# Performance work log

Measured on AMD Instinct MI355X. Metric: run time of the kernel, lower is better.

Reference implementation:

```python
import jax, jax.numpy as jnp
import numpy as np

B, N = 4, 1024            # batches, atoms per structure
IN_CH, OUT_CH = 16, 16
N_BASIS = 16
MAX_RADIUS = 3.5
BOX_L = 19.7              # cubic lattice constant -> ~24 neighbors/atom
GAMMA = MAX_RADIUS / N_BASIS
N_NORM = 24.0             # avg neighbor count, out /= sqrt(n_norm)


def _build_periodic_edges(seed=0):
    rng = np.random.default_rng(seed)
    pos = rng.uniform(0.0, BOX_L, (B, N, 3)).astype(np.float32)
    shifts = BOX_L * np.array([[i, j, k] for i in (-1, 0, 1)
                               for j in (-1, 0, 1) for k in (-1, 0, 1)],
                              dtype=np.float32)
    src_l, dst_l, vec_l = [], [], []
    r2 = MAX_RADIUS * MAX_RADIUS
    for z in range(B):
        p = pos[z]
        for s in shifts:  # 27 periodic images, chunked to keep memory small
            diff = (p[None, :, :] + s[None, None, :]) - p[:, None, :]  # [a,b,3] = image_b - a
            d2 = (diff * diff).sum(-1)
            a_idx, b_idx = np.nonzero(d2 < r2)
            dst_l.append((z * N + a_idx).astype(np.int32))
            src_l.append((z * N + b_idx).astype(np.int32))
            vec_l.append(diff[a_idx, b_idx])
    edge_src = np.concatenate(src_l)
    edge_dst = np.concatenate(dst_l)
    edge_vec = np.concatenate(vec_l).astype(np.float32)
    # original zeroes self-image displacements with |r| < 1e-10
    self_mask = np.linalg.norm(edge_vec, axis=-1) < 1e-10
    edge_vec[self_mask] = 0.0
    return edge_src, edge_dst, edge_vec


def setup_inputs() -> dict:
    key = jax.random.key(0)
    k1, k2 = jax.random.split(key)
    edge_src, edge_dst, edge_vec = _build_periodic_edges()
    x = jax.random.normal(k1, (B * N, IN_CH), dtype=jnp.float32)
    W = jax.random.normal(k2, (N_BASIS + 3, OUT_CH, IN_CH), dtype=jnp.float32) * 0.1
    return {
        "x": x,
        "W": W,
        "edge_vec": jnp.asarray(edge_vec),
        "edge_src": jnp.asarray(edge_src),
        "edge_dst": jnp.asarray(edge_dst),
    }


def reference(x, W, edge_vec, edge_src, edge_dst):
    # per-edge kernel features: gaussian radial basis + unit direction
    r = jnp.linalg.norm(edge_vec, axis=-1, keepdims=True)            # [E,1]
    centers = jnp.linspace(0.0, MAX_RADIUS, N_BASIS, dtype=x.dtype)
    basis = jnp.exp(-((r - centers) / GAMMA) ** 2)                   # [E,nb]
    rhat = jnp.where(r > 1e-10, edge_vec / jnp.maximum(r, 1e-10), 0.0)
    feat = jnp.concatenate([basis, rhat], axis=-1)                   # [E,nb+3]
    # per-edge kernel eval (kernels = self.kernel(radius) in the original)
    K = jnp.einsum('ef,foi->eoi', feat, W)                           # [E,out,in]
    # per-edge matvec + scatter-add over destination atoms
    msg = jnp.einsum('eoi,ei->eo', K, x[edge_src])                   # [E,out]
    out = jax.ops.segment_sum(msg, edge_dst, num_segments=x.shape[0])
    out = out / jnp.sqrt(jnp.asarray(N_NORM, x.dtype))               # n_norm ** 0.5
    return out.reshape(B, N, OUT_CH)
```

## Files before the change

kernel.cpp:

```cpp
#include <hip/hip_runtime.h>
#include <hip/hip_fp16.h>
#include <math.h>

#define IN_CH 16
#define OUT_CH 16
#define N_BASIS 16
#define N_FEAT 19
#define Y_STRIDE (N_FEAT * OUT_CH)
#define GAMMA_INV (16.0f / 3.5f)
#define CENTER_STEP (3.5f / 15.0f)
#define INV_SQRT_NNORM 0.20412414523193154f
#define APB 16
#define EPB 32

__global__ __launch_bounds__(320) void precompute_y(
    const float* __restrict__ x, const float* __restrict__ W,
    __half* __restrict__ y, float* __restrict__ out, int n_atoms) {
  __shared__ float xs[APB][IN_CH];
  const int t = threadIdx.x;
  const int a0 = blockIdx.x * APB;

  if (t < APB * IN_CH) {
    const int idx = a0 * IN_CH + t;
    const bool ok = idx < n_atoms * IN_CH;
    xs[t >> 4][t & 15] = ok ? x[idx] : 0.0f;
    if (ok) out[idx] = 0.0f;
  }

  float4 w0, w1, w2, w3;
  if (t < Y_STRIDE) {
    const float4* w4 = (const float4*)(W + t * IN_CH);
    w0 = w4[0]; w1 = w4[1]; w2 = w4[2]; w3 = w4[3];
  }
  __syncthreads();

  if (t < Y_STRIDE) {
#pragma unroll
    for (int al = 0; al < APB; ++al) {
      if (a0 + al >= n_atoms) break;
      const float* xv = xs[al];
      float acc = w0.x * xv[0] + w0.y * xv[1] + w0.z * xv[2] + w0.w * xv[3] +
                  w1.x * xv[4] + w1.y * xv[5] + w1.z * xv[6] + w1.w * xv[7] +
                  w2.x * xv[8] + w2.y * xv[9] + w2.z * xv[10] + w2.w * xv[11] +
                  w3.x * xv[12] + w3.y * xv[13] + w3.z * xv[14] + w3.w * xv[15];
      y[(size_t)(a0 + al) * Y_STRIDE + t] = __float2half(acc * INV_SQRT_NNORM);
    }
  }
}

__global__ __launch_bounds__(256) void edge_scatter(
    const __half* __restrict__ y, const float* __restrict__ edge_vec,
    const int* __restrict__ edge_src, const int* __restrict__ edge_dst,
    float* __restrict__ out, int E) {
  __shared__ float feat[EPB][20];
  __shared__ float msg[EPB][OUT_CH];
  __shared__ int dsts[EPB];

  const int t = threadIdx.x;
  const int w = t >> 7;
  const int rem = t & 127;
  const int el = rem & 15;
  const int h = rem >> 4;
  const int s = w * 16 + el;
  const int e = blockIdx.x * EPB + s;
  const bool valid = (e < E);

  float vx = 0.f, vy = 0.f, vz = 0.f;
  int src = 0;
  if (valid) {
    vx = edge_vec[3 * e + 0];
    vy = edge_vec[3 * e + 1];
    vz = edge_vec[3 * e + 2];
    src = edge_src[e];
    if (h == 0) dsts[s] = edge_dst[e];
  } else if (h == 0) {
    dsts[s] = -1 - s;
  }
  const float r = sqrtf(vx * vx + vy * vy + vz * vz);

  const float t0 = (r - CENTER_STEP * (float)(2 * h)) * GAMMA_INV;
  const float t1 = (r - CENTER_STEP * (float)(2 * h + 1)) * GAMMA_INV;
  feat[s][2 * h] = __expf(-t0 * t0);
  feat[s][2 * h + 1] = __expf(-t1 * t1);
  if (h < 3) {
    const float inv = (r > 1e-10f) ? (1.0f / r) : 0.0f;
    const float comp = (h == 0) ? vx : ((h == 1) ? vy : vz);
    feat[s][N_BASIS + h] = comp * inv;
  }
  __syncthreads();

  float a0 = 0.f, a1 = 0.f;
  if (valid) {
    const __half2* __restrict__ yrow =
        (const __half2*)(y + (size_t)src * Y_STRIDE + 2 * h);
#pragma unroll
    for (int f = 0; f < N_FEAT; ++f) {
      const float2 yv = __half22float2(yrow[f * (OUT_CH / 2)]);
      const float ff = feat[s][f];
      a0 += ff * yv.x;
      a1 += ff * yv.y;
    }
  }
  msg[s][2 * h] = a0;
  msg[s][2 * h + 1] = a1;
  __syncthreads();

  const int wb = w * 16;
  const int mydst = dsts[s];
  int leader = el;
#pragma unroll
  for (int k = 0; k < 16; ++k) {
    if (dsts[wb + k] == mydst) { leader = k; break; }
  }
  if (leader == el && mydst >= 0) {
    float s0 = 0.f, s1 = 0.f;
#pragma unroll
    for (int k = 0; k < 16; ++k) {
      if (k >= el && dsts[wb + k] == mydst) {
        s0 += msg[wb + k][2 * h];
        s1 += msg[wb + k][2 * h + 1];
      }
    }
    atomicAdd(&out[mydst * OUT_CH + 2 * h], s0);
    atomicAdd(&out[mydst * OUT_CH + 2 * h + 1], s1);
  }
}

__global__ __launch_bounds__(256) void edge_direct(
    const float* __restrict__ x, const float* __restrict__ W,
    const float* __restrict__ edge_vec, const int* __restrict__ edge_src,
    const int* __restrict__ edge_dst, float* __restrict__ out, int E) {
  __shared__ float Ws[N_FEAT * OUT_CH * IN_CH];
  __shared__ float feat[16][N_FEAT];
  __shared__ float xs[16][IN_CH];

  const int t = threadIdx.x;
  for (int i = t; i < N_FEAT * OUT_CH * IN_CH; i += 256) Ws[i] = W[i];

  const int eg = t >> 4;
  const int o = t & 15;
  const int e = blockIdx.x * 16 + eg;
  const bool valid = (e < E);

  float vx = 0.f, vy = 0.f, vz = 0.f;
  int src = 0, dst = 0;
  if (valid) {
    vx = edge_vec[3 * e + 0];
    vy = edge_vec[3 * e + 1];
    vz = edge_vec[3 * e + 2];
    src = edge_src[e];
    dst = edge_dst[e];
    xs[eg][o] = x[src * IN_CH + o];
  }
  const float r = sqrtf(vx * vx + vy * vy + vz * vz);
  const float tt = (r - CENTER_STEP * (float)o) * GAMMA_INV;
  feat[eg][o] = __expf(-tt * tt);
  if (o < 3) {
    const float inv = (r > 1e-10f) ? (1.0f / r) : 0.0f;
    const float comp = (o == 0) ? vx : ((o == 1) ? vy : vz);
    feat[eg][N_BASIS + o] = comp * inv;
  }
  __syncthreads();

  if (valid) {
    float acc = 0.f;
#pragma unroll
    for (int f = 0; f < N_FEAT; ++f) {
      const float* wrow = &Ws[(f * OUT_CH + o) * IN_CH];
      float dot = 0.f;
#pragma unroll
      for (int i = 0; i < IN_CH; ++i) dot += wrow[i] * xs[eg][i];
      acc += feat[eg][f] * dot;
    }
    atomicAdd(&out[dst * OUT_CH + o], acc * INV_SQRT_NNORM);
  }
}

extern "C" void kernel_launch(void* const* d_in, const int* in_sizes, int n_in,
                              void* d_out, int out_size, void* d_ws,
                              size_t ws_size, hipStream_t stream) {
  const float* x = (const float*)d_in[0];
  const float* W = (const float*)d_in[1];
  const float* edge_vec = (const float*)d_in[2];
  const int* edge_src = (const int*)d_in[3];
  const int* edge_dst = (const int*)d_in[4];
  float* out = (float*)d_out;

  const int E = in_sizes[3];
  const int n_atoms = in_sizes[0] / IN_CH;

  const size_t y_bytes = (size_t)n_atoms * Y_STRIDE * sizeof(__half);
  if (ws_size >= y_bytes) {
    __half* y = (__half*)d_ws;
    precompute_y<<<(n_atoms + APB - 1) / APB, 320, 0, stream>>>(x, W, y, out,
                                                               n_atoms);
    edge_scatter<<<(E + EPB - 1) / EPB, 256, 0, stream>>>(y, edge_vec, edge_src,
                                                          edge_dst, out, E);
  } else {
    hipMemsetAsync(out, 0, (size_t)out_size * sizeof(float), stream);
    edge_direct<<<(E + 15) / 16, 256, 0, stream>>>(x, W, edge_vec, edge_src,
                                                   edge_dst, out, E);
  }
}
```

Measured before the change: 90.31 us.

## Use one atom per block in precompute and remap edge_scatter thread layout

The precompute kernel now launches one block per atom instead of batching 16 atoms per block, so each block reloads the W row through global memory and uses less per-block reuse. In edge_scatter the thread-to-(edge, output pair) mapping is swapped so that the 8 output-pair threads of one edge are adjacent. The y-row reads per edge become contiguous within a wavefront, and messages are stored as float2. This trades better coalescing of the gathered y rows against more blocks and more redundant W loads in the precompute.

```diff
diff --git a/kernel.cpp b/kernel.cpp
--- a/kernel.cpp
+++ b/kernel.cpp
@@ -10,41 +10,29 @@
 #define GAMMA_INV (16.0f / 3.5f)
 #define CENTER_STEP (3.5f / 15.0f)
 #define INV_SQRT_NNORM 0.20412414523193154f
-#define APB 16
 #define EPB 32
 
 __global__ __launch_bounds__(320) void precompute_y(
     const float* __restrict__ x, const float* __restrict__ W,
-    __half* __restrict__ y, float* __restrict__ out, int n_atoms) {
-  __shared__ float xs[APB][IN_CH];
+    __half* __restrict__ y, float* __restrict__ out) {
+  __shared__ float xs[IN_CH];
+  const int a = blockIdx.x;
   const int t = threadIdx.x;
-  const int a0 = blockIdx.x * APB;
-
-  if (t < APB * IN_CH) {
-    const int idx = a0 * IN_CH + t;
-    const bool ok = idx < n_atoms * IN_CH;
-    xs[t >> 4][t & 15] = ok ? x[idx] : 0.0f;
-    if (ok) out[idx] = 0.0f;
+  if (t < IN_CH) {
+    xs[t] = x[a * IN_CH + t];
+    out[a * OUT_CH + t] = 0.0f;
   }
-
-  float4 w0, w1, w2, w3;
+  __syncthreads();
   if (t < Y_STRIDE) {
     const float4* w4 = (const float4*)(W + t * IN_CH);
-    w0 = w4[0]; w1 = w4[1]; w2 = w4[2]; w3 = w4[3];
-  }
-  __syncthreads();
-
-  if (t < Y_STRIDE) {
+    float acc = 0.f;
 #pragma unroll
-    for (int al = 0; al < APB; ++al) {
-      if (a0 + al >= n_atoms) break;
-      const float* xv = xs[al];
-      float acc = w0.x * xv[0] + w0.y * xv[1] + w0.z * xv[2] + w0.w * xv[3] +
-                  w1.x * xv[4] + w1.y * xv[5] + w1.z * xv[6] + w1.w * xv[7] +
-                  w2.x * xv[8] + w2.y * xv[9] + w2.z * xv[10] + w2.w * xv[11] +
-                  w3.x * xv[12] + w3.y * xv[13] + w3.z * xv[14] + w3.w * xv[15];
-      y[(size_t)(a0 + al) * Y_STRIDE + t] = __float2half(acc * INV_SQRT_NNORM);
+    for (int q = 0; q < 4; ++q) {
+      float4 w = w4[q];
+      acc += w.x * xs[4 * q + 0] + w.y * xs[4 * q + 1] +
+             w.z * xs[4 * q + 2] + w.w * xs[4 * q + 3];
     }
+    y[(size_t)a * Y_STRIDE + t] = __float2half(acc * INV_SQRT_NNORM);
   }
 }
 
@@ -53,14 +41,13 @@
     const int* __restrict__ edge_src, const int* __restrict__ edge_dst,
     float* __restrict__ out, int E) {
   __shared__ float feat[EPB][20];
-  __shared__ float msg[EPB][OUT_CH];
+  __shared__ float2 msg2[EPB][8];
   __shared__ int dsts[EPB];
 
   const int t = threadIdx.x;
+  const int h = t & 7;
+  const int el = (t >> 3) & 15;
   const int w = t >> 7;
-  const int rem = t & 127;
-  const int el = rem & 15;
-  const int h = rem >> 4;
   const int s = w * 16 + el;
   const int e = blockIdx.x * EPB + s;
   const bool valid = (e < E);
@@ -101,8 +88,7 @@
       a1 += ff * yv.y;
     }
   }
-  msg[s][2 * h] = a0;
-  msg[s][2 * h + 1] = a1;
+  msg2[s][h] = make_float2(a0, a1);
   __syncthreads();
 
   const int wb = w * 16;
@@ -117,8 +103,9 @@
 #pragma unroll
     for (int k = 0; k < 16; ++k) {
       if (k >= el && dsts[wb + k] == mydst) {
-        s0 += msg[wb + k][2 * h];
-        s1 += msg[wb + k][2 * h + 1];
+        const float2 m = msg2[wb + k][h];
+        s0 += m.x;
+        s1 += m.y;
       }
     }
     atomicAdd(&out[mydst * OUT_CH + 2 * h], s0);
@@ -192,8 +179,7 @@
   const size_t y_bytes = (size_t)n_atoms * Y_STRIDE * sizeof(__half);
   if (ws_size >= y_bytes) {
     __half* y = (__half*)d_ws;
-    precompute_y<<<(n_atoms + APB - 1) / APB, 320, 0, stream>>>(x, W, y, out,
-                                                               n_atoms);
+    precompute_y<<<n_atoms, 320, 0, stream>>>(x, W, y, out);
     edge_scatter<<<(E + EPB - 1) / EPB, 256, 0, stream>>>(y, edge_vec, edge_src,
                                                           edge_dst, out, E);
   } else {
```

Measured after the change: 78.62 us. -13.0%, faster.

## Give each edge-scatter thread four output channels and double edges per block

Applied to the files above, without the earlier changes.

The edge scatter kernel now gives each thread four output channels instead of two, so four threads cover one edge and a 256-thread block handles 64 edges instead of 32. Each thread loads 8 bytes of half-precision y per feature, and messages are staged in shared memory as float4. The thread mapping changes so that the 4 channel-threads of one edge are adjacent lanes, which should improve gather coalescing and cut redundant per-edge loads and radius computation. In exchange each thread does more serial work, issues more atomics, and there are fewer threads per edge, so less parallelism is available.

```diff
diff --git a/kernel.cpp b/kernel.cpp
--- a/kernel.cpp
+++ b/kernel.cpp
@@ -11,7 +11,7 @@
 #define CENTER_STEP (3.5f / 15.0f)
 #define INV_SQRT_NNORM 0.20412414523193154f
 #define APB 16
-#define EPB 32
+#define EPB 64
 
 __global__ __launch_bounds__(320) void precompute_y(
     const float* __restrict__ x, const float* __restrict__ W,
@@ -53,14 +53,13 @@
     const int* __restrict__ edge_src, const int* __restrict__ edge_dst,
     float* __restrict__ out, int E) {
   __shared__ float feat[EPB][20];
-  __shared__ float msg[EPB][OUT_CH];
+  __shared__ float4 msg4[EPB][4];
   __shared__ int dsts[EPB];
 
   const int t = threadIdx.x;
-  const int w = t >> 7;
-  const int rem = t & 127;
-  const int el = rem & 15;
-  const int h = rem >> 4;
+  const int h = t & 3;
+  const int el = (t >> 2) & 15;
+  const int w = t >> 6;
   const int s = w * 16 + el;
   const int e = blockIdx.x * EPB + s;
   const bool valid = (e < E);
@@ -78,10 +77,11 @@
   }
   const float r = sqrtf(vx * vx + vy * vy + vz * vz);
 
-  const float t0 = (r - CENTER_STEP * (float)(2 * h)) * GAMMA_INV;
-  const float t1 = (r - CENTER_STEP * (float)(2 * h + 1)) * GAMMA_INV;
-  feat[s][2 * h] = __expf(-t0 * t0);
-  feat[s][2 * h + 1] = __expf(-t1 * t1);
+#pragma unroll
+  for (int j = 0; j < 4; ++j) {
+    const float tb = (r - CENTER_STEP * (float)(4 * h + j)) * GAMMA_INV;
+    feat[s][4 * h + j] = __expf(-tb * tb);
+  }
   if (h < 3) {
     const float inv = (r > 1e-10f) ? (1.0f / r) : 0.0f;
     const float comp = (h == 0) ? vx : ((h == 1) ? vy : vz);
@@ -89,20 +89,25 @@
   }
   __syncthreads();
 
-  float a0 = 0.f, a1 = 0.f;
-  if (valid) {
-    const __half2* __restrict__ yrow =
-        (const __half2*)(y + (size_t)src * Y_STRIDE + 2 * h);
+  float a0 = 0.f, a1 = 0.f, a2 = 0.f, a3 = 0.f;
+  if (valid) {
+    const float2* __restrict__ yrow =
+        (const float2*)(y + (size_t)src * Y_STRIDE + 4 * h);
 #pragma unroll
     for (int f = 0; f < N_FEAT; ++f) {
-      const float2 yv = __half22float2(yrow[f * (OUT_CH / 2)]);
+      const float2 raw = yrow[f * (OUT_CH / 4)];
+      const __half2 p0 = *(const __half2*)&raw.x;
+      const __half2 p1 = *(const __half2*)&raw.y;
+      const float2 v0 = __half22float2(p0);
+      const float2 v1 = __half22float2(p1);
       const float ff = feat[s][f];
-      a0 += ff * yv.x;
-      a1 += ff * yv.y;
-    }
-  }
-  msg[s][2 * h] = a0;
-  msg[s][2 * h + 1] = a1;
+      a0 += ff * v0.x;
+      a1 += ff * v0.y;
+      a2 += ff * v1.x;
+      a3 += ff * v1.y;
+    }
+  }
+  msg4[s][h] = make_float4(a0, a1, a2, a3);
   __syncthreads();
 
   const int wb = w * 16;
@@ -113,16 +118,19 @@
     if (dsts[wb + k] == mydst) { leader = k; break; }
   }
   if (leader == el && mydst >= 0) {
-    float s0 = 0.f, s1 = 0.f;
+    float s0 = 0.f, s1 = 0.f, s2 = 0.f, s3 = 0.f;
 #pragma unroll
     for (int k = 0; k < 16; ++k) {
       if (k >= el && dsts[wb + k] == mydst) {
-        s0 += msg[wb + k][2 * h];
-        s1 += msg[wb + k][2 * h + 1];
+        const float4 m = msg4[wb + k][h];
+        s0 += m.x; s1 += m.y; s2 += m.z; s3 += m.w;
       }
     }
-    atomicAdd(&out[mydst * OUT_CH + 2 * h], s0);
-    atomicAdd(&out[mydst * OUT_CH + 2 * h + 1], s1);
+    float* base = &out[mydst * OUT_CH + 4 * h];
+    atomicAdd(base + 0, s0);
+    atomicAdd(base + 1, s1);
+    atomicAdd(base + 2, s2);
+    atomicAdd(base + 3, s3);
   }
 }
 
```

Result: faster. 76.59 us (median of 2 runs) (-15.2%).
